# Performance work log

Measured on AMD Instinct MI355X. Metric: run time of the kernel, lower is better.

The kernel has to match this reference:

```python
import jax, jax.numpy as jnp
import numpy as np

INPUT_DIMS = 512
OUTPUT_DIMS = 512
GRID_SIZE = 8


def setup_inputs() -> dict:
    key = jax.random.key(0)
    k_x, k_w = jax.random.split(key)
    x = jax.random.normal(k_x, (4, 2048, INPUT_DIMS), dtype=jnp.float32)
    scale = 1.0 / (np.sqrt(INPUT_DIMS) * np.sqrt(GRID_SIZE))
    fouriercoeffs = jax.random.normal(
        k_w, (2, OUTPUT_DIMS, INPUT_DIMS, GRID_SIZE), dtype=jnp.float32) * scale
    bias = jnp.zeros((1, OUTPUT_DIMS), dtype=jnp.float32)
    return {"x": x, "fouriercoeffs": fouriercoeffs, "bias": bias}


def reference(x, fouriercoeffs, bias):
    out_shape = x.shape[:-1] + (OUTPUT_DIMS,)
    xf = x.reshape(-1, INPUT_DIMS)  # [N, I]
    k = jnp.arange(1, GRID_SIZE + 1, dtype=x.dtype)  # [G]
    arg = xf[:, :, None] * k  # [N, I, G]
    # contract cos/sin features against coeffs: two batched GEMMs
    y = jnp.einsum('nig,oig->no', jnp.cos(arg), fouriercoeffs[0])
    y = y + jnp.einsum('nig,oig->no', jnp.sin(arg), fouriercoeffs[1])
    y = y + bias
    return y.reshape(out_shape)
```

## Files before the change

kernel.cpp:

```cpp
#include <hip/hip_runtime.h>
#include <hip/hip_bf16.h>


typedef __attribute__((ext_vector_type(8)))  short s16x8;
typedef __attribute__((ext_vector_type(4)))  int   i32x4;
typedef __attribute__((ext_vector_type(4)))  float f32x4;
typedef __attribute__((ext_vector_type(16))) float f32x16;

#define NROWS 8192
#define IDIM  512
#define ODIM  512
#define KDIM  8192

static __device__ __forceinline__ short f2bf(float f) {
    union { float f; unsigned u; } v; v.f = f;
    unsigned r = v.u + 0x7fffu + ((v.u >> 16) & 1u);
    return (short)(r >> 16);
}

static __device__ __forceinline__ float bf2f(short h) {
    union { unsigned u; float f; } v;
    v.u = ((unsigned)(unsigned short)h) << 16;
    return v.f;
}

static __device__ __forceinline__ int pkbf(float c, float s) {
    union { __hip_bfloat162 h; int i; } u;
    u.h = __float22bfloat162_rn(make_float2(c, s));
    return u.i;
}

__global__ __launch_bounds__(256) void fkan_prep(const float* __restrict__ cf,
                                                 short* __restrict__ Wb) {
    const int o = blockIdx.x;
    const int tid = threadIdx.x;
#pragma unroll
    for (int rep = 0; rep < 2; ++rep) {
        const int i = tid + rep * 256;
        const float* c0 = cf + (o * 512 + i) * 8;
        const float* c1 = cf + ((512 + o) * 512 + i) * 8;
        float4 a0 = *(const float4*)c0;
        float4 a1 = *(const float4*)(c0 + 4);
        float4 b0 = *(const float4*)c1;
        float4 b1 = *(const float4*)(c1 + 4);
        s16x8 lo, hi;
        lo[0] = f2bf(a0.x); lo[1] = f2bf(b0.x);
        lo[2] = f2bf(a0.y); lo[3] = f2bf(b0.y);
        lo[4] = f2bf(a0.z); lo[5] = f2bf(b0.z);
        lo[6] = f2bf(a0.w); lo[7] = f2bf(b0.w);
        hi[0] = f2bf(a1.x); hi[1] = f2bf(b1.x);
        hi[2] = f2bf(a1.y); hi[3] = f2bf(b1.y);
        hi[4] = f2bf(a1.z); hi[5] = f2bf(b1.z);
        hi[6] = f2bf(a1.w); hi[7] = f2bf(b1.w);
        *(s16x8*)(Wb + o * KDIM + i * 16)     = lo;
        *(s16x8*)(Wb + o * KDIM + i * 16 + 8) = hi;
    }
}

__global__ __launch_bounds__(512, 2) void fkan_gemm15(const float* __restrict__ x,
                                                      const short* __restrict__ Wb,
                                                      short* __restrict__ P) {
    __shared__ short As[2][256 * 40];
    __shared__ short Bs[2][128 * 64];

    const int bid = blockIdx.x;
    const int xcd = bid & 7;
    const int bn = xcd & 1, kc = xcd >> 1;
    const int bm = bid >> 3;
    const int n0 = bm * 256, o0 = bn * 256, i0 = kc * 128;
    const int kbase = i0 * 16;
    const int NKT = 64;

    const int tid = threadIdx.x;
    const int wid = tid >> 6, lane = tid & 63;
    const int l32 = lane & 31, hi32 = lane >> 5;
    const int wr = wid >> 2, wc = wid & 3;

    f32x16 acc[4][2];
#pragma unroll
    for (int a = 0; a < 4; ++a)
#pragma unroll
        for (int b = 0; b < 2; ++b)
#pragma unroll
            for (int e = 0; e < 16; ++e) acc[a][b][e] = 0.f;

    const int nl = tid >> 1, isel = tid & 1;
    const float* xrow = x + (size_t)(n0 + nl) * 512 + i0 + isel;
    const int sAo = nl * 40 + isel * 16;

    auto stage = [&](int t, int nb, float xx) {
#pragma unroll
        for (int w = 0; w < 2; ++w) {
            const int ch = w * 512 + tid;
            const int l = ch >> 3, sl = ch & 7;
            const int cb = sl ^ (l & 7);
            const int r = 2 * l + (cb >> 2);
            const short* src = Wb + (size_t)(o0 + r) * KDIM + kbase + t * 32 + (cb & 3) * 8;
            short* ldst = &Bs[nb][w * 4096 + wid * 512];
            __builtin_amdgcn_global_load_lds(
                (const __attribute__((address_space(1))) void*)src,
                (__attribute__((address_space(3))) void*)ldst, 16, 0, 0);
        }
        float s1, c1;
        __sincosf(xx, &s1, &c1);
        float c = c1, s = s1;
        i32x4 lo, hi;
#pragma unroll
        for (int g = 0; g < 8; ++g) {
            const int p = pkbf(c, s);
            if (g < 4) lo[g] = p; else hi[g - 4] = p;
            const float t1 = s * s1, t2 = c * s1;
            const float cn = __builtin_fmaf(c, c1, -t1);
            s = __builtin_fmaf(s, c1, t2);
            c = cn;
        }
        short* Ab = As[nb];
        *(i32x4*)&Ab[sAo]     = lo;
        *(i32x4*)&Ab[sAo + 8] = hi;
    };

    float xv = xrow[0];
    stage(0, 0, xv);
    xv = xrow[2];
    __syncthreads();

    for (int kt = 0; kt < NKT; ++kt) {
        const int cur = kt & 1;

        s16x8 af[4][2], bfr[2][2];
#pragma unroll
        for (int mt = 0; mt < 4; ++mt)
#pragma unroll
            for (int ks = 0; ks < 2; ++ks) {
                const int row = wr * 128 + mt * 32 + l32;
                af[mt][ks] = *(const s16x8*)&As[cur][row * 40 + (ks * 2 + hi32) * 8];
            }
#pragma unroll
        for (int nt = 0; nt < 2; ++nt)
#pragma unroll
            for (int ks = 0; ks < 2; ++ks) {
                const int row = wc * 64 + nt * 32 + l32;
                const int l = row >> 1;
                const int slot = (((row & 1) * 4 + ks * 2 + hi32) ^ (l & 7));
                bfr[nt][ks] = *(const s16x8*)&Bs[cur][l * 64 + slot * 8];
            }

        if (kt + 1 < NKT) {
            stage(kt + 1, cur ^ 1, xv);
            if (kt + 2 < NKT) xv = xrow[(kt + 2) * 2];
        }

#pragma unroll
        for (int ks = 0; ks < 2; ++ks)
#pragma unroll
            for (int mt = 0; mt < 4; ++mt)
#pragma unroll
                for (int nt = 0; nt < 2; ++nt)
                    acc[mt][nt] = __builtin_amdgcn_mfma_f32_32x32x16_bf16(
                        af[mt][ks], bfr[nt][ks], acc[mt][nt], 0, 0, 0);

        __syncthreads();
    }

    unsigned short* dst = (unsigned short*)P + (size_t)kc * (NROWS * ODIM);
#pragma unroll
    for (int mt = 0; mt < 4; ++mt)
#pragma unroll
        for (int nt = 0; nt < 2; ++nt) {
            const f32x16 v = acc[mt][nt];
            const int oc = o0 + wc * 64 + nt * 32 + l32;
            const int rb = n0 + wr * 128 + mt * 32 + 4 * hi32;
#pragma unroll
            for (int reg = 0; reg < 16; ++reg) {
                const int row = rb + (reg & 3) + 8 * (reg >> 2);
                dst[(size_t)row * 512 + oc] = (unsigned short)f2bf(v[reg]);
            }
        }
}

__global__ __launch_bounds__(256) void fkan_combine4(const short* __restrict__ P,
                                                     const float* __restrict__ bias,
                                                     float* __restrict__ out) {
    const int total = NROWS * ODIM;
    const int stride = gridDim.x * 256 * 8;
    for (int e = (blockIdx.x * 256 + threadIdx.x) * 8; e < total; e += stride) {
        s16x8 a = *(const s16x8*)(P + e);
        s16x8 b = *(const s16x8*)(P + total + e);
        s16x8 c = *(const s16x8*)(P + 2 * total + e);
        s16x8 d = *(const s16x8*)(P + 3 * total + e);
        const int col = e & 511;
        float4 c0 = *(const float4*)(bias + col);
        float4 c1 = *(const float4*)(bias + col + 4);
        float4 r0, r1;
        r0.x = (bf2f(a[0]) + bf2f(b[0])) + (bf2f(c[0]) + bf2f(d[0])) + c0.x;
        r0.y = (bf2f(a[1]) + bf2f(b[1])) + (bf2f(c[1]) + bf2f(d[1])) + c0.y;
        r0.z = (bf2f(a[2]) + bf2f(b[2])) + (bf2f(c[2]) + bf2f(d[2])) + c0.z;
        r0.w = (bf2f(a[3]) + bf2f(b[3])) + (bf2f(c[3]) + bf2f(d[3])) + c0.w;
        r1.x = (bf2f(a[4]) + bf2f(b[4])) + (bf2f(c[4]) + bf2f(d[4])) + c1.x;
        r1.y = (bf2f(a[5]) + bf2f(b[5])) + (bf2f(c[5]) + bf2f(d[5])) + c1.y;
        r1.z = (bf2f(a[6]) + bf2f(b[6])) + (bf2f(c[6]) + bf2f(d[6])) + c1.z;
        r1.w = (bf2f(a[7]) + bf2f(b[7])) + (bf2f(c[7]) + bf2f(d[7])) + c1.w;
        *(float4*)(out + e)     = r0;
        *(float4*)(out + e + 4) = r1;
    }
}

__global__ __launch_bounds__(256, 2) void fkan_gemm_fb(const float* __restrict__ x,
                                                       const short* __restrict__ Wb,
                                                       const float* __restrict__ bias,
                                                       float* __restrict__ outp) {
    __shared__ short As[2][128 * 64];
    __shared__ short Bs[2][128 * 64];
    const int bid = blockIdx.x;
    const int xcd = bid & 7, idx = bid >> 3;
    const int bn = xcd & 3, bm = idx + (xcd >> 2) * 32;
    const int n0 = bm * 128, o0 = bn * 128;
    const int tid = threadIdx.x;
    const int wid = tid >> 6, lane = tid & 63;
    const int lrow = lane & 15, lk = lane >> 4;
    const int wr = wid >> 1, wc = wid & 1;
    f32x4 acc[4][4];
#pragma unroll
    for (int a = 0; a < 4; ++a)
#pragma unroll
        for (int b = 0; b < 4; ++b) { f32x4 z = {0,0,0,0}; acc[a][b] = z; }
    const int nl = tid >> 1, isel = tid & 1;
    const float* xrow = x + (n0 + nl) * 512 + isel * 2;
    auto stage = [&](int t, int nb, float2 xvv) {
#pragma unroll
        for (int w = 0; w < 4; ++w) {
            const int chunk = w * 256 + tid;
            const int r = chunk >> 3, pc = chunk & 7;
            const int lc = pc ^ (r & 7);
            const short* src = Wb + (o0 + r) * KDIM + t * 64 + lc * 8;
            short* ldst = &Bs[nb][w * 2048 + wid * 512];
            __builtin_amdgcn_global_load_lds(
                (const __attribute__((address_space(1))) void*)src,
                (__attribute__((address_space(3))) void*)ldst, 16, 0, 0);
        }
#pragma unroll
        for (int ii = 0; ii < 2; ++ii) {
            const float xx = ii ? xvv.y : xvv.x;
            float s1, c1; __sincosf(xx, &s1, &c1);
            float c = c1, s = s1;
            i32x4 lo, hi;
#pragma unroll
            for (int g = 0; g < 8; ++g) {
                const int p = pkbf(c, s);
                if (g < 4) lo[g] = p; else hi[g - 4] = p;
                const float t1 = s * s1, t2 = c * s1;
                const float cn = __builtin_fmaf(c, c1, -t1);
                s = __builtin_fmaf(s, c1, t2); c = cn;
            }
            const int cb0 = (isel * 2 + ii) * 2;
            *(i32x4*)&As[nb][nl * 64 + ((cb0 ^ (nl & 7))) * 8]       = lo;
            *(i32x4*)&As[nb][nl * 64 + (((cb0 + 1) ^ (nl & 7))) * 8] = hi;
        }
    };
    float2 xv = *(const float2*)xrow;
    stage(0, 0, xv);
    xv = *(const float2*)(xrow + 4);
    __syncthreads();
    for (int kt = 0; kt < 128; ++kt) {
        const int cur = kt & 1;
        s16x8 af[2][4], bfr[2][4];
#pragma unroll
        for (int ksub = 0; ksub < 2; ++ksub) {
#pragma unroll
            for (int mf = 0; mf < 4; ++mf) {
                const int row = wr * 64 + mf * 16 + lrow;
                af[ksub][mf] = *(const s16x8*)&As[cur][row * 64 + ((ksub * 4 + lk) ^ (row & 7)) * 8];
            }
#pragma unroll
            for (int nf = 0; nf < 4; ++nf) {
                const int row = wc * 64 + nf * 16 + lrow;
                bfr[ksub][nf] = *(const s16x8*)&Bs[cur][row * 64 + ((ksub * 4 + lk) ^ (row & 7)) * 8];
            }
        }
        if (kt + 1 < 128) {
            stage(kt + 1, cur ^ 1, xv);
            if (kt + 2 < 128) xv = *(const float2*)(xrow + (kt + 2) * 4);
        }
#pragma unroll
        for (int ksub = 0; ksub < 2; ++ksub)
#pragma unroll
            for (int mf = 0; mf < 4; ++mf)
#pragma unroll
                for (int nf = 0; nf < 4; ++nf)
                    acc[mf][nf] = __builtin_amdgcn_mfma_f32_16x16x32_bf16(
                        af[ksub][mf], bfr[ksub][nf], acc[mf][nf], 0, 0, 0);
        __syncthreads();
    }
#pragma unroll
    for (int nf = 0; nf < 4; ++nf) {
        const int oc = o0 + wc * 64 + nf * 16 + lrow;
        const float bv = bias[oc];
#pragma unroll
        for (int mf = 0; mf < 4; ++mf) {
            const f32x4 v = acc[mf][nf];
            const int rbase = n0 + wr * 64 + mf * 16 + lk * 4;
#pragma unroll
            for (int j = 0; j < 4; ++j)
                outp[(size_t)(rbase + j) * 512 + oc] = v[j] + bv;
        }
    }
}

extern "C" void kernel_launch(void* const* d_in, const int* in_sizes, int n_in,
                              void* d_out, int out_size, void* d_ws, size_t ws_size,
                              hipStream_t stream) {
    const float* x    = (const float*)d_in[0];
    const float* cf   = (const float*)d_in[1];
    const float* bias = (const float*)d_in[2];
    float* out = (float*)d_out;

    const size_t partial_bytes = (size_t)4 * NROWS * ODIM * 2;
    const size_t wb_bytes = (size_t)ODIM * KDIM * 2;

    if (ws_size >= partial_bytes + wb_bytes) {
        short* P  = (short*)d_ws;
        short* Wb = (short*)((char*)d_ws + partial_bytes);
        fkan_prep<<<512, 256, 0, stream>>>(cf, Wb);
        fkan_gemm15<<<256, 512, 0, stream>>>(x, Wb, P);
        fkan_combine4<<<2048, 256, 0, stream>>>(P, bias, out);
    } else {
        short* Wb = (short*)d_ws;
        fkan_prep<<<512, 256, 0, stream>>>(cf, Wb);
        fkan_gemm_fb<<<256, 256, 0, stream>>>(x, Wb, bias, out);
    }
}
```

Measured before the change: 90.67 us.

## Double K-tile depth and interleave staging with per-quarter MFMA groups

The GEMM kernel's K-tile grows from 32 to 64 (NT halves to 32 iterations), with LDS A and B buffers enlarged. Each tile is split into four quarter-phases, and the B global-to-LDS loads and the two sin/cos A-feature computations are spread across those phases. Explicit s_barrier, waitcnt and setprio calls keep MFMA runs back to back. The aim is fewer barriers per unit of K and better overlap of feature generation and loads with matrix math, at the cost of more LDS per block (possibly reducing occupancy) and fragile hand-placed waitcnt logic.

```diff
diff --git a/kernel.cpp b/kernel.cpp
--- a/kernel.cpp
+++ b/kernel.cpp
@@ -57,11 +57,11 @@
     }
 }
 
-__global__ __launch_bounds__(512, 2) void fkan_gemm15(const float* __restrict__ x,
+__global__ __launch_bounds__(512, 2) void fkan_gemm16(const float* __restrict__ x,
                                                       const short* __restrict__ Wb,
                                                       short* __restrict__ P) {
-    __shared__ short As[2][256 * 40];
-    __shared__ short Bs[2][128 * 64];
+    __shared__ short As[2][256 * 72];
+    __shared__ short Bs[2][256 * 64];
 
     const int bid = blockIdx.x;
     const int xcd = bid & 7;
@@ -69,7 +69,7 @@
     const int bm = bid >> 3;
     const int n0 = bm * 256, o0 = bn * 256, i0 = kc * 128;
     const int kbase = i0 * 16;
-    const int NKT = 64;
+    const int NT = 32;
 
     const int tid = threadIdx.x;
     const int wid = tid >> 6, lane = tid & 63;
@@ -84,23 +84,24 @@
 #pragma unroll
             for (int e = 0; e < 16; ++e) acc[a][b][e] = 0.f;
 
-    const int nl = tid >> 1, isel = tid & 1;
-    const float* xrow = x + (size_t)(n0 + nl) * 512 + i0 + isel;
-    const int sAo = nl * 40 + isel * 16;
-
-    auto stage = [&](int t, int nb, float xx) {
-#pragma unroll
-        for (int w = 0; w < 2; ++w) {
+    const int arow_s = tid >> 1, hsel = tid & 1;
+    const float* xptr = x + (size_t)(n0 + arow_s) * 512 + i0 + 2 * hsel;
+    float2 xv;
+
+    auto stageB = [&](int t, short* Bw) {
+#pragma unroll
+        for (int w = 0; w < 4; ++w) {
             const int ch = w * 512 + tid;
             const int l = ch >> 3, sl = ch & 7;
             const int cb = sl ^ (l & 7);
-            const int r = 2 * l + (cb >> 2);
-            const short* src = Wb + (size_t)(o0 + r) * KDIM + kbase + t * 32 + (cb & 3) * 8;
-            short* ldst = &Bs[nb][w * 4096 + wid * 512];
+            const short* src = Wb + (size_t)(o0 + l) * KDIM + kbase + t * 64 + cb * 8;
+            short* ldst = Bw + w * 4096 + wid * 512;
             __builtin_amdgcn_global_load_lds(
                 (const __attribute__((address_space(1))) void*)src,
                 (__attribute__((address_space(3))) void*)ldst, 16, 0, 0);
         }
+    };
+    auto stageA1 = [&](short* Aw, float xx, int j) {
         float s1, c1;
         __sincosf(xx, &s1, &c1);
         float c = c1, s = s1;
@@ -114,52 +115,73 @@
             s = __builtin_fmaf(s, c1, t2);
             c = cn;
         }
-        short* Ab = As[nb];
-        *(i32x4*)&Ab[sAo]     = lo;
-        *(i32x4*)&Ab[sAo + 8] = hi;
+        const int il = 2 * hsel + j;
+        *(i32x4*)&Aw[arow_s * 72 + il * 16]     = lo;
+        *(i32x4*)&Aw[arow_s * 72 + il * 16 + 8] = hi;
     };
 
-    float xv = xrow[0];
-    stage(0, 0, xv);
-    xv = xrow[2];
-    __syncthreads();
-
-    for (int kt = 0; kt < NKT; ++kt) {
-        const int cur = kt & 1;
-
-        s16x8 af[4][2], bfr[2][2];
-#pragma unroll
-        for (int mt = 0; mt < 4; ++mt)
-#pragma unroll
-            for (int ks = 0; ks < 2; ++ks) {
-                const int row = wr * 128 + mt * 32 + l32;
-                af[mt][ks] = *(const s16x8*)&As[cur][row * 40 + (ks * 2 + hi32) * 8];
-            }
-#pragma unroll
-        for (int nt = 0; nt < 2; ++nt)
-#pragma unroll
-            for (int ks = 0; ks < 2; ++ks) {
-                const int row = wc * 64 + nt * 32 + l32;
-                const int l = row >> 1;
-                const int slot = (((row & 1) * 4 + ks * 2 + hi32) ^ (l & 7));
-                bfr[nt][ks] = *(const s16x8*)&Bs[cur][l * 64 + slot * 8];
-            }
-
-        if (kt + 1 < NKT) {
-            stage(kt + 1, cur ^ 1, xv);
-            if (kt + 2 < NKT) xv = xrow[(kt + 2) * 2];
-        }
-
-#pragma unroll
-        for (int ks = 0; ks < 2; ++ks)
-#pragma unroll
-            for (int mt = 0; mt < 4; ++mt)
+    auto group = [&](int t, const short* Ar, const short* Br,
+                     short* Aw, short* Bw, bool stg, bool ldx) {
+        s16x8 bfr[2][4];
+#pragma unroll
+        for (int q = 0; q < 4; ++q) {
+            if (q == 0) {
 #pragma unroll
                 for (int nt = 0; nt < 2; ++nt)
-                    acc[mt][nt] = __builtin_amdgcn_mfma_f32_32x32x16_bf16(
-                        af[mt][ks], bfr[nt][ks], acc[mt][nt], 0, 0, 0);
-
-        __syncthreads();
+#pragma unroll
+                    for (int kk = 0; kk < 4; ++kk) {
+                        const int row = wc * 64 + nt * 32 + l32;
+                        const int cb = kk * 2 + hi32;
+                        bfr[nt][kk] = *(const s16x8*)&Br[row * 64 + (cb ^ (row & 7)) * 8];
+                    }
+            }
+            s16x8 af[4];
+            {
+                const int row = wr * 128 + q * 32 + l32;
+#pragma unroll
+                for (int kk = 0; kk < 4; ++kk)
+                    af[kk] = *(const s16x8*)&Ar[row * 72 + (kk * 2 + hi32) * 8];
+            }
+            if (q == 0 && stg) stageB(t + 1, Bw);
+            if (q == 1 && stg) stageA1(Aw, xv.x, 0);
+            if (q == 2 && stg) stageA1(Aw, xv.y, 1);
+            if (q == 3) {
+                if (ldx) xv = *(const float2*)(xptr + (t + 2) * 4);
+                if (ldx)      asm volatile("s_waitcnt vmcnt(1)" ::: "memory");
+                else if (stg) asm volatile("s_waitcnt vmcnt(0)" ::: "memory");
+                __builtin_amdgcn_sched_barrier(0);
+            }
+            __builtin_amdgcn_s_barrier();
+            asm volatile("s_waitcnt lgkmcnt(0)" ::: "memory");
+            __builtin_amdgcn_sched_barrier(0);
+            __builtin_amdgcn_s_setprio(1);
+#pragma unroll
+            for (int kk = 0; kk < 4; ++kk)
+#pragma unroll
+                for (int nt = 0; nt < 2; ++nt)
+                    acc[q][nt] = __builtin_amdgcn_mfma_f32_32x32x16_bf16(
+                        af[kk], bfr[nt][kk], acc[q][nt], 0, 0, 0);
+            __builtin_amdgcn_s_setprio(0);
+            __builtin_amdgcn_s_barrier();
+        }
+    };
+
+    {
+        float2 x0 = *(const float2*)(xptr);
+        stageB(0, Bs[0]);
+        stageA1(As[0], x0.x, 0);
+        stageA1(As[0], x0.y, 1);
+        xv = *(const float2*)(xptr + 4);
+        asm volatile("s_waitcnt vmcnt(1) lgkmcnt(0)" ::: "memory");
+        __builtin_amdgcn_sched_barrier(0);
+        __builtin_amdgcn_s_barrier();
+    }
+
+#pragma unroll 1
+    for (int tp = 0; tp < 16; ++tp) {
+        const int t0 = tp * 2;
+        group(t0,     As[0], Bs[0], As[1], Bs[1], true,          t0 + 2 < NT);
+        group(t0 + 1, As[1], Bs[1], As[0], Bs[0], t0 + 2 < NT,   t0 + 3 < NT);
     }
 
     unsigned short* dst = (unsigned short*)P + (size_t)kc * (NROWS * ODIM);
@@ -321,7 +343,7 @@
         short* P  = (short*)d_ws;
         short* Wb = (short*)((char*)d_ws + partial_bytes);
         fkan_prep<<<512, 256, 0, stream>>>(cf, Wb);
-        fkan_gemm15<<<256, 512, 0, stream>>>(x, Wb, P);
+        fkan_gemm16<<<256, 512, 0, stream>>>(x, Wb, P);
         fkan_combine4<<<2048, 256, 0, stream>>>(P, bias, out);
     } else {
         short* Wb = (short*)d_ws;
```

After: 98.78 us. +8.9%, slower.
